# Kernel tuning notes

Hardware: AMD Instinct MI355X
Metric: run time of the kernel (lower is better)

Reference implementation:

```python
import jax, jax.numpy as jnp
import numpy as np

N, EN, NNZ, D, H = 100000, 25000, 200000, 128, 4
F = D  # out_channels per head (out_channels == embed_dim)
NEG_SLOPE = 0.2


def segment_softmax(logits, seg, num_segments):
    # numerically stable softmax over entries sharing the same segment id
    m = jax.ops.segment_max(logits, seg, num_segments=num_segments)
    ex = jnp.exp(logits - m[seg])
    s = jax.ops.segment_sum(ex, seg, num_segments=num_segments)
    return ex / s[seg]


def setup_inputs():
    key = jax.random.key(0)
    ks = jax.random.split(key, 10)
    X = jax.random.normal(ks[0], (N, D), jnp.float32)
    E = jax.random.normal(ks[1], (EN, D), jnp.float32)
    row = jax.random.randint(ks[2], (NNZ,), 0, N, dtype=jnp.int32)
    col = (jnp.arange(NNZ, dtype=jnp.int32) % EN)  # every hyperedge non-empty
    adj_index = jnp.stack([row, col])  # [2, nnz]
    adj_values = jax.random.uniform(ks[3], (NNZ,), jnp.float32) + 0.1
    s = 1.0 / np.sqrt(D)
    Wn = jax.random.normal(ks[4], (D, D), jnp.float32) * s
    bn = jnp.zeros((D,), jnp.float32)
    We = jax.random.normal(ks[5], (D, D), jnp.float32) * s
    be = jnp.zeros((D,), jnp.float32)
    Wlin = jax.random.normal(ks[6], (D, H * F), jnp.float32) * s
    att = jax.random.normal(ks[7], (1, H, 2 * F), jnp.float32) * s
    bias_conv = jnp.zeros((F,), jnp.float32)
    return {"X": X, "E": E, "adj_index": adj_index, "adj_values": adj_values,
            "Wn": Wn, "bn": bn, "We": We, "be": be, "Wlin": Wlin,
            "att": att, "bias_conv": bias_conv}


def reference(X, E, adj_index, adj_values, Wn, bn, We, be, Wlin, att, bias_conv):
    row, col = adj_index[0], adj_index[1]  # node idx, hyperedge idx

    # ---- compute_edge_feat: E_res = B^{-1} A^T (X Wn + bn) + (E We + be) + E
    edge_deg = jax.ops.segment_sum(adj_values, col, num_segments=EN)  # tsp.sum(A,0)
    norm_factor = 1.0 / edge_deg  # edges guaranteed non-empty
    X_trans = X @ Wn + bn
    agg = jax.ops.segment_sum(adj_values[:, None] * X_trans[row], col, num_segments=EN)
    E_res = norm_factor[:, None] * agg + (E @ We + be) + E

    # ---- HypergraphConv(use_attention=True, heads=H, concat=False), eval (dropout off)
    x = (X @ Wlin).reshape(N, H, F)
    e = (E_res @ Wlin).reshape(EN, H, F)
    x_i = x[row]           # [nnz, H, F]
    e_j = e[col]           # [nnz, H, F]
    alpha = (x_i * att[:, :, :F]).sum(-1) + (e_j * att[:, :, F:]).sum(-1)  # [nnz, H]
    alpha = jax.nn.leaky_relu(alpha, NEG_SLOPE)
    alpha = segment_softmax(alpha, row, N)  # softmax grouped by node index

    # degree normalizations D (nodes) and B (hyperedges)
    Dn = jax.ops.segment_sum(adj_values[col], row, num_segments=N)
    Dn = jnp.where(Dn > 0, 1.0 / Dn, 0.0)
    Bn = jax.ops.segment_sum(jnp.ones((NNZ,), x.dtype), col, num_segments=EN)
    Bn = jnp.where(Bn > 0, 1.0 / Bn, 0.0)

    # node -> hyperedge aggregation
    m1 = Bn[col][:, None, None] * x_i * alpha[:, :, None]
    out_e = jax.ops.segment_sum(m1, col, num_segments=EN)  # [EN, H, F]
    # hyperedge -> node aggregation
    m2 = Dn[row][:, None, None] * out_e[col] * alpha[:, :, None]
    out_n = jax.ops.segment_sum(m2, row, num_segments=N)   # [N, H, F]

    X_res = out_n.mean(axis=1) + bias_conv  # concat=False -> mean over heads + bias
    return (X_res, E_res)
```

## Files before the change

kernel.cpp:

```cpp
#include <hip/hip_runtime.h>

#define NN 100000
#define ENUM 25000
#define NNZ_C 200000

typedef __attribute__((ext_vector_type(8))) short bf16x8;
typedef __attribute__((ext_vector_type(4))) float f32x4;

__device__ __forceinline__ float blo(unsigned u) { return __uint_as_float(u << 16); }
__device__ __forceinline__ float bhi(unsigned u) { return __uint_as_float(u & 0xFFFF0000u); }
__device__ __forceinline__ unsigned short f2bf(float x) {
    unsigned u = __float_as_uint(x);
    unsigned r = (u + 0x7fff + ((u >> 16) & 1)) >> 16;
    return (unsigned short)r;
}
__device__ __forceinline__ unsigned pack2(float a, float b) {
    return (unsigned)f2bf(a) | ((unsigned)f2bf(b) << 16);
}
__device__ __forceinline__ void gload_lds16(const unsigned short* g, unsigned short* l) {
    __builtin_amdgcn_global_load_lds(
        (const __attribute__((address_space(1))) void*)g,
        (__attribute__((address_space(3))) void*)l, 16, 0, 0);
}

__global__ __launch_bounds__(256) void wtr_k(
    const float* __restrict__ W, unsigned short* __restrict__ Wt, int NC)
{
    const int t = blockIdx.x * 256 + threadIdx.x;
    if (t >= 128 * NC) return;
    const int c = t % NC, k = t / NC;
    const size_t pos = ((size_t)c * 128 + k) ^ ((c & 7) << 3);
    Wt[pos] = f2bf(W[t]);
}

__global__ __launch_bounds__(256) void wtr_big_k(
    const float* __restrict__ Wlin, unsigned short* __restrict__ WbigT)
{
    const int t = blockIdx.x * 256 + threadIdx.x;
    if (t >= 128 * 512) return;
    const int d = t >> 9, c512 = t & 511;
    const int h = c512 >> 7, f = c512 & 127;
    const int kk = d * 4 + h;
    const int kc = kk >> 7, dd = kk & 127;
    const size_t pos = (size_t)kc * 16384 + (((size_t)f * 128 + dd) ^ ((f & 7) << 3));
    WbigT[pos] = f2bf(Wlin[t]);
}

__global__ __launch_bounds__(256) void attw_k(
    const float* __restrict__ Wlin, const float* __restrict__ att,
    const float* __restrict__ bn, const float* __restrict__ be,
    float* __restrict__ A1, float* __restrict__ A2, float* __restrict__ bnbe)
{
    const int t = threadIdx.x;
    const int k = t & 127;
    const int pair = t >> 7;
    const float* wrow = Wlin + (size_t)k * 512;
    float s[4];
    #pragma unroll
    for (int h = 0; h < 4; h++) {
        float acc = 0.f;
        const float* ap = att + h * 256 + pair * 128;
        const float* wp = wrow + h * 128;
        for (int f = 0; f < 128; f++) acc += wp[f] * ap[f];
        s[h] = acc;
    }
    float* dst = (pair ? A2 : A1) + k * 4;
    dst[0] = s[0]; dst[1] = s[1]; dst[2] = s[2]; dst[3] = s[3];
    if (t < 128) bnbe[t] = bn[t] + be[t];
}

__global__ __launch_bounds__(256) void ax_k(
    const float* __restrict__ X, const float* __restrict__ A1,
    float* __restrict__ ax, int M)
{
    const int r = blockIdx.x * 4 + (threadIdx.x >> 6);
    const int lane = threadIdx.x & 63;
    if (r >= M) return;
    const int f0 = lane * 2;
    const float2 x = *(const float2*)(X + (size_t)r * 128 + f0);
    const float4 a0 = *(const float4*)(A1 + f0 * 4);
    const float4 a1 = *(const float4*)(A1 + f0 * 4 + 4);
    float s0 = x.x * a0.x + x.y * a1.x;
    float s1 = x.x * a0.y + x.y * a1.y;
    float s2 = x.x * a0.z + x.y * a1.z;
    float s3 = x.x * a0.w + x.y * a1.w;
    #pragma unroll
    for (int off = 1; off < 64; off <<= 1) {
        s0 += __shfl_xor(s0, off); s1 += __shfl_xor(s1, off);
        s2 += __shfl_xor(s2, off); s3 += __shfl_xor(s3, off);
    }
    if (lane == 0) *(float4*)(ax + (size_t)r * 4) = make_float4(s0, s1, s2, s3);
}

__global__ __launch_bounds__(256) void agg_k(
    const int* __restrict__ row, const float* __restrict__ adjv,
    const float* __restrict__ X, unsigned short* __restrict__ agg)
{
    const int e = blockIdx.x * 4 + (threadIdx.x >> 6);
    const int lane = threadIdx.x & 63;
    if (e >= ENUM) return;
    const int f0 = lane * 2;
    float a0 = 0.f, a1 = 0.f, deg = 0.f;
    #pragma unroll
    for (int j = 0; j < 8; j++) {
        const int k = e + j * ENUM;
        const float w = adjv[k];
        deg += w;
        const float2 x = *(const float2*)(X + (size_t)row[k] * 128 + f0);
        a0 += w * x.x; a1 += w * x.y;
    }
    const float rs = 1.f / deg;
    ((unsigned*)agg)[(size_t)e * 64 + lane] = pack2(a0 * rs, a1 * rs);
}

__global__ __launch_bounds__(256) void gemme_k(
    const unsigned short* __restrict__ agg, const float* __restrict__ E,
    const unsigned short* __restrict__ WnT, const unsigned short* __restrict__ WeT,
    const float* __restrict__ bnbe, float* __restrict__ Eres, int M)
{
    __shared__ unsigned short Ag[64 * 128];
    __shared__ unsigned short Ae[64 * 128];
    __shared__ unsigned short Bw[64 * 128];
    __shared__ unsigned short Bv[64 * 128];
    const int tid = threadIdx.x;
    const int r0 = blockIdx.x * 64;

    {
        int rr = tid >> 4;
        const int kc = (tid & 15) * 8;
        #pragma unroll
        for (int it = 0; it < 4; it++) {
            int r = r0 + rr; if (r > M - 1) r = M - 1;
            const uint4 vg = *(const uint4*)(agg + (size_t)r * 128 + kc);
            const float* ep = E + (size_t)r * 128 + kc;
            const float4 f0 = *(const float4*)ep;
            const float4 f1 = *(const float4*)(ep + 4);
            uint4 ve;
            ve.x = pack2(f0.x, f0.y); ve.y = pack2(f0.z, f0.w);
            ve.z = pack2(f1.x, f1.y); ve.w = pack2(f1.z, f1.w);
            const int idx = (rr * 128 + kc) ^ ((rr & 7) << 3);
            *(uint4*)&Ag[idx] = vg;
            *(uint4*)&Ae[idx] = ve;
            rr += 16;
        }
    }
    __syncthreads();

    const int lane = tid & 63;
    const int wid = tid >> 6;
    const int wr = wid >> 1, wc = wid & 1;
    const int fr = lane & 15;
    const int kg = (lane >> 4) * 8;

    bf16x8 ag[2][4], ae_[2][4];
    #pragma unroll
    for (int m = 0; m < 2; m++) {
        const int ar = wr * 32 + m * 16 + fr;
        #pragma unroll
        for (int ks = 0; ks < 4; ks++) {
            const int idx = (ar * 128 + ks * 32 + kg) ^ ((ar & 7) << 3);
            ag[m][ks] = *(const bf16x8*)&Ag[idx];
            ae_[m][ks] = *(const bf16x8*)&Ae[idx];
        }
    }

    for (int ct = 0; ct < 2; ct++) {
        __syncthreads();
        {
            const unsigned short* s1 = WnT + (size_t)ct * 8192 + tid * 8;
            const unsigned short* s2 = WeT + (size_t)ct * 8192 + tid * 8;
            unsigned short* d1 = &Bw[tid * 8];
            unsigned short* d2 = &Bv[tid * 8];
            #pragma unroll
            for (int it = 0; it < 4; it++) {
                gload_lds16(s1 + it * 2048, d1 + it * 2048);
                gload_lds16(s2 + it * 2048, d2 + it * 2048);
            }
        }
        __syncthreads();

        f32x4 acc[2][2] = {};
        #pragma unroll
        for (int ks = 0; ks < 4; ks++) {
            bf16x8 bw[2], bv[2];
            #pragma unroll
            for (int n = 0; n < 2; n++) {
                const int br = wc * 32 + n * 16 + fr;
                const int idx = (br * 128 + ks * 32 + kg) ^ ((br & 7) << 3);
                bw[n] = *(const bf16x8*)&Bw[idx];
                bv[n] = *(const bf16x8*)&Bv[idx];
            }
            #pragma unroll
            for (int m = 0; m < 2; m++)
                #pragma unroll
                for (int n = 0; n < 2; n++) {
                    acc[m][n] = __builtin_amdgcn_mfma_f32_16x16x32_bf16(ag[m][ks], bw[n], acc[m][n], 0, 0, 0);
                    acc[m][n] = __builtin_amdgcn_mfma_f32_16x16x32_bf16(ae_[m][ks], bv[n], acc[m][n], 0, 0, 0);
                }
        }

        #pragma unroll
        for (int m = 0; m < 2; m++) {
            #pragma unroll
            for (int n = 0; n < 2; n++) {
                const int c = ct * 64 + wc * 32 + n * 16 + fr;
                #pragma unroll
                for (int j = 0; j < 4; j++) {
                    const int r = r0 + wr * 32 + m * 16 + (lane >> 4) * 4 + j;
                    if (r < M)
                        Eres[(size_t)r * 128 + c] = acc[m][n][j] + bnbe[c] + E[(size_t)r * 128 + c];
                }
            }
        }
    }
}

__global__ __launch_bounds__(256) void ae_k(
    const float* __restrict__ Eres, const float* __restrict__ A2,
    float* __restrict__ ae)
{
    const int e = blockIdx.x * 4 + (threadIdx.x >> 6);
    const int lane = threadIdx.x & 63;
    if (e >= ENUM) return;
    const int f0 = lane * 2;
    const float2 v = *(const float2*)(Eres + (size_t)e * 128 + f0);
    const float4 a0 = *(const float4*)(A2 + f0 * 4);
    const float4 a1 = *(const float4*)(A2 + f0 * 4 + 4);
    float s0 = v.x * a0.x + v.y * a1.x;
    float s1 = v.x * a0.y + v.y * a1.y;
    float s2 = v.x * a0.z + v.y * a1.z;
    float s3 = v.x * a0.w + v.y * a1.w;
    #pragma unroll
    for (int off = 1; off < 64; off <<= 1) {
        s0 += __shfl_xor(s0, off); s1 += __shfl_xor(s1, off);
        s2 += __shfl_xor(s2, off); s3 += __shfl_xor(s3, off);
    }
    if (lane == 0) *(float4*)(ae + (size_t)e * 4) = make_float4(s0, s1, s2, s3);
}

__global__ __launch_bounds__(256) void zero_k(unsigned* __restrict__ p, int n)
{
    const int t = blockIdx.x * 256 + threadIdx.x;
    if (t < n) p[t] = 0u;
}

__global__ __launch_bounds__(256) void hist_k(
    const int* __restrict__ row, int* __restrict__ cnt)
{
    const int k = blockIdx.x * 256 + threadIdx.x;
    if (k < NNZ_C) atomicAdd(cnt + row[k], 1);
}

__global__ __launch_bounds__(256) void scan1_k(
    const int* __restrict__ cnt, int* __restrict__ rp, int* __restrict__ bsum, int n)
{
    __shared__ int sh[256];
    const int t = threadIdx.x, g = blockIdx.x * 256 + t;
    const int v = (g < n) ? cnt[g] : 0;
    sh[t] = v; __syncthreads();
    #pragma unroll
    for (int off = 1; off < 256; off <<= 1) {
        const int add = (t >= off) ? sh[t - off] : 0;
        __syncthreads();
        sh[t] += add;
        __syncthreads();
    }
    if (g < n) rp[g] = sh[t] - v;
    if (t == 255) bsum[blockIdx.x] = sh[255];
}

__global__ __launch_bounds__(512) void scan2_k(int* __restrict__ bsum, int nb)
{
    __shared__ int sh[512];
    const int t = threadIdx.x;
    const int v = (t < nb) ? bsum[t] : 0;
    sh[t] = v; __syncthreads();
    #pragma unroll
    for (int off = 1; off < 512; off <<= 1) {
        const int add = (t >= off) ? sh[t - off] : 0;
        __syncthreads();
        sh[t] += add;
        __syncthreads();
    }
    if (t < nb) bsum[t] = sh[t] - v;
}

__global__ __launch_bounds__(256) void scan3_k(
    int* __restrict__ rp, const int* __restrict__ bsum, int* __restrict__ cur, int n)
{
    const int g = blockIdx.x * 256 + threadIdx.x;
    if (g < n) {
        const int v = rp[g] + bsum[g >> 8];
        rp[g] = v;
        cur[g] = v;
    }
    if (g == 0) rp[n] = NNZ_C;
}

__global__ __launch_bounds__(256) void fill_k(
    const int* __restrict__ row, int* __restrict__ cur, int* __restrict__ eidx)
{
    const int k = blockIdx.x * 256 + threadIdx.x;
    if (k < NNZ_C) {
        const int p = atomicAdd(cur + row[k], 1);
        eidx[p] = k;
    }
}

__global__ __launch_bounds__(256) void softmax_csr_k(
    const int* __restrict__ rowptr, const int* __restrict__ eidx,
    const float* __restrict__ ax, const float* __restrict__ ae,
    float* __restrict__ alpha, float* __restrict__ alphag)
{
    const int r = blockIdx.x * 256 + threadIdx.x;
    if (r >= NN) return;
    const int p0 = rowptr[r], p1 = rowptr[r + 1];
    if (p0 == p1) return;
    const float4 axv = *(const float4*)(ax + (size_t)r * 4);

#define LRELU4(a) { a.x = (a.x >= 0.f) ? a.x : 0.2f * a.x;                    \
                    a.y = (a.y >= 0.f) ? a.y : 0.2f * a.y;                    \
                    a.z = (a.z >= 0.f) ? a.z : 0.2f * a.z;                    \
                    a.w = (a.w >= 0.f) ? a.w : 0.2f * a.w; }

    float4 m = make_float4(-1e30f, -1e30f, -1e30f, -1e30f);
    for (int p = p0; p < p1; ++p) {
        const int c = eidx[p] % ENUM;
        float4 a = *(const float4*)(ae + (size_t)c * 4);
        a.x += axv.x; a.y += axv.y; a.z += axv.z; a.w += axv.w;
        LRELU4(a);
        m.x = fmaxf(m.x, a.x); m.y = fmaxf(m.y, a.y);
        m.z = fmaxf(m.z, a.z); m.w = fmaxf(m.w, a.w);
    }
    float4 s = make_float4(0.f, 0.f, 0.f, 0.f);
    for (int p = p0; p < p1; ++p) {
        const int c = eidx[p] % ENUM;
        float4 a = *(const float4*)(ae + (size_t)c * 4);
        a.x += axv.x; a.y += axv.y; a.z += axv.z; a.w += axv.w;
        LRELU4(a);
        s.x += __expf(a.x - m.x); s.y += __expf(a.y - m.y);
        s.z += __expf(a.z - m.z); s.w += __expf(a.w - m.w);
    }
    const float4 rs = make_float4(1.f / s.x, 1.f / s.y, 1.f / s.z, 1.f / s.w);
    for (int p = p0; p < p1; ++p) {
        const int k = eidx[p];
        const int c = k % ENUM;
        float4 a = *(const float4*)(ae + (size_t)c * 4);
        a.x += axv.x; a.y += axv.y; a.z += axv.z; a.w += axv.w;
        LRELU4(a);
        float4 v;
        v.x = __expf(a.x - m.x) * rs.x; v.y = __expf(a.y - m.y) * rs.y;
        v.z = __expf(a.z - m.z) * rs.z; v.w = __expf(a.w - m.w) * rs.w;
        *(float4*)(alpha + ((size_t)k << 2)) = v;
        *(float4*)(alphag + ((size_t)p << 2)) = v;
    }
#undef LRELU4
}

__global__ __launch_bounds__(256) void aggx_k(
    const int* __restrict__ row, const float* __restrict__ alpha,
    const float* __restrict__ X, unsigned short* __restrict__ aggX)
{
    const int e = blockIdx.x * 4 + (threadIdx.x >> 6);
    const int lane = threadIdx.x & 63;
    if (e >= ENUM) return;
    const int f0 = lane * 2;
    float d0h0 = 0.f, d0h1 = 0.f, d0h2 = 0.f, d0h3 = 0.f;
    float d1h0 = 0.f, d1h1 = 0.f, d1h2 = 0.f, d1h3 = 0.f;
    #pragma unroll
    for (int j = 0; j < 8; j++) {
        const int k = e + j * ENUM;
        const float4 al = *(const float4*)(alpha + ((size_t)k << 2));
        const float2 x = *(const float2*)(X + (size_t)row[k] * 128 + f0);
        d0h0 += al.x * x.x; d0h1 += al.y * x.x; d0h2 += al.z * x.x; d0h3 += al.w * x.x;
        d1h0 += al.x * x.y; d1h1 += al.y * x.y; d1h2 += al.z * x.y; d1h3 += al.w * x.y;
    }
    uint4 o;
    o.x = pack2(0.125f * d0h0, 0.125f * d0h1);
    o.y = pack2(0.125f * d0h2, 0.125f * d0h3);
    o.z = pack2(0.125f * d1h0, 0.125f * d1h1);
    o.w = pack2(0.125f * d1h2, 0.125f * d1h3);
    *(uint4*)(aggX + (size_t)e * 512 + f0 * 4) = o;
}

__global__ __launch_bounds__(256) void aggn_k(
    const int* __restrict__ rowptr, const int* __restrict__ eidx,
    const float* __restrict__ adjv, const float* __restrict__ alphag,
    const unsigned short* __restrict__ aggX, unsigned short* __restrict__ aggN)
{
    const int r = blockIdx.x * 4 + (threadIdx.x >> 6);
    const int lane = threadIdx.x & 63;
    if (r >= NN) return;
    const int p0 = rowptr[r], p1 = rowptr[r + 1];
    const int f0 = lane * 2;
    float d0h0 = 0.f, d0h1 = 0.f, d0h2 = 0.f, d0h3 = 0.f;
    float d1h0 = 0.f, d1h1 = 0.f, d1h2 = 0.f, d1h3 = 0.f;
    float ds = 0.f;

#define AGN_BODY(P) {                                                         \
        const int c = eidx[P] % ENUM;                                         \
        ds += adjv[c];                                                        \
        const float4 al = *(const float4*)(alphag + ((size_t)(P) << 2));      \
        const uint4 u = *(const uint4*)(aggX + (size_t)c * 512 + f0 * 4);     \
        d0h0 += al.x * blo(u.x); d0h1 += al.y * bhi(u.x);                     \
        d0h2 += al.z * blo(u.y); d0h3 += al.w * bhi(u.y);                     \
        d1h0 += al.x * blo(u.z); d1h1 += al.y * bhi(u.z);                     \
        d1h2 += al.z * blo(u.w); d1h3 += al.w * bhi(u.w);                     \
    }

    int p = p0;
    for (; p + 2 <= p1; p += 2) { AGN_BODY(p); AGN_BODY(p + 1); }
    if (p < p1) AGN_BODY(p);
#undef AGN_BODY

    const float w = (p1 > p0) ? 0.25f / ds : 0.f;
    uint4 o;
    o.x = pack2(w * d0h0, w * d0h1);
    o.y = pack2(w * d0h2, w * d0h3);
    o.z = pack2(w * d1h0, w * d1h1);
    o.w = pack2(w * d1h2, w * d1h3);
    *(uint4*)(aggN + (size_t)r * 512 + f0 * 4) = o;
}

__global__ __launch_bounds__(256) void gemmf_k(
    const unsigned short* __restrict__ aggN, const unsigned short* __restrict__ WbigT,
    const float* __restrict__ bias, float* __restrict__ Xres, int M)
{
    __shared__ unsigned short As[64 * 128];
    __shared__ unsigned short Bs[128 * 128];
    const int tid = threadIdx.x;
    const int r0 = blockIdx.x * 64;
    const int lane = tid & 63;
    const int w = tid >> 6;
    const int wr = w >> 1, wc = w & 1;
    const int fr = lane & 15;
    const int kg = (lane >> 4) * 8;

    f32x4 acc[2][4] = {};

    for (int kc = 0; kc < 4; kc++) {
        __syncthreads();
        {
            int rr = tid >> 4;
            const int kcol = (tid & 15) * 8;
            #pragma unroll
            for (int it = 0; it < 4; it++) {
                int r = r0 + rr; if (r > M - 1) r = M - 1;
                const uint4 va = *(const uint4*)(aggN + (size_t)r * 512 + kc * 128 + kcol);
                *(uint4*)&As[(rr * 128 + kcol) ^ ((rr & 7) << 3)] = va;
                rr += 16;
            }
        }
        {
            const unsigned short* src = WbigT + (size_t)kc * 16384 + tid * 8;
            unsigned short* dst = &Bs[tid * 8];
            #pragma unroll
            for (int it = 0; it < 8; it++)
                gload_lds16(src + it * 2048, dst + it * 2048);
        }
        __syncthreads();

        #pragma unroll
        for (int ks = 0; ks < 4; ks++) {
            bf16x8 a[2], b[4];
            #pragma unroll
            for (int m = 0; m < 2; m++) {
                const int ar = wr * 32 + m * 16 + fr;
                a[m] = *(const bf16x8*)&As[(ar * 128 + ks * 32 + kg) ^ ((ar & 7) << 3)];
            }
            #pragma unroll
            for (int n = 0; n < 4; n++) {
                const int br = wc * 64 + n * 16 + fr;
                b[n] = *(const bf16x8*)&Bs[(br * 128 + ks * 32 + kg) ^ ((br & 7) << 3)];
            }
            #pragma unroll
            for (int m = 0; m < 2; m++)
                #pragma unroll
                for (int n = 0; n < 4; n++)
                    acc[m][n] = __builtin_amdgcn_mfma_f32_16x16x32_bf16(a[m], b[n], acc[m][n], 0, 0, 0);
        }
    }

    #pragma unroll
    for (int m = 0; m < 2; m++) {
        #pragma unroll
        for (int n = 0; n < 4; n++) {
            const int c = wc * 64 + n * 16 + fr;
            #pragma unroll
            for (int j = 0; j < 4; j++) {
                const int r = r0 + wr * 32 + m * 16 + (lane >> 4) * 4 + j;
                if (r < M)
                    Xres[(size_t)r * 128 + c] = acc[m][n][j] + bias[c];
            }
        }
    }
}

extern "C" void kernel_launch(void* const* d_in, const int* in_sizes, int n_in,
                              void* d_out, int out_size, void* d_ws, size_t ws_size,
                              hipStream_t stream)
{
    const float* X         = (const float*)d_in[0];
    const float* E         = (const float*)d_in[1];
    const int*   adj       = (const int*)d_in[2];
    const float* adjv      = (const float*)d_in[3];
    const float* Wn        = (const float*)d_in[4];
    const float* bn        = (const float*)d_in[5];
    const float* We        = (const float*)d_in[6];
    const float* be        = (const float*)d_in[7];
    const float* Wlin      = (const float*)d_in[8];
    const float* att       = (const float*)d_in[9];
    const float* bias_conv = (const float*)d_in[10];
    const int* row = adj;

    float* Xres = (float*)d_out;
    float* Eres = Xres + (size_t)NN * 128;

    char* wsb = (char*)d_ws;
    unsigned short* aggX  = (unsigned short*)(wsb);
    unsigned short* agg   = (unsigned short*)(wsb + 25600000);
    unsigned short* aggN  = (unsigned short*)(wsb + 51200000);
    unsigned short* WbigT = (unsigned short*)(wsb + 153600000);
    unsigned short* WnT   = (unsigned short*)(wsb + 153731072);
    unsigned short* WeT   = (unsigned short*)(wsb + 153763840);
    float* A1    = (float*)(wsb + 153796608);
    float* A2    = (float*)(wsb + 153798656);
    float* bnbe  = (float*)(wsb + 153800704);
    float* ax    = (float*)(wsb + 153802752);
    float* ae    = (float*)(wsb + 155402752);
    float* alpha = (float*)(wsb + 155802752);
    int* rowptr  = (int*)(wsb + 159002752);
    int* cnt     = (int*)(wsb + 159402768);
    int* eidx    = (int*)(wsb + 159802768);
    int* bsum    = (int*)(wsb + 160602768);
    float* alphag= (float*)(wsb + 160604816);

    zero_k<<<(NN + 255) / 256, 256, 0, stream>>>((unsigned*)cnt, NN);
    hist_k<<<(NNZ_C + 255) / 256, 256, 0, stream>>>(row, cnt);
    scan1_k<<<(NN + 255) / 256, 256, 0, stream>>>(cnt, rowptr, bsum, NN);
    scan2_k<<<1, 512, 0, stream>>>(bsum, (NN + 255) / 256);
    scan3_k<<<(NN + 255) / 256, 256, 0, stream>>>(rowptr, bsum, cnt, NN);
    fill_k<<<(NNZ_C + 255) / 256, 256, 0, stream>>>(row, cnt, eidx);

    wtr_big_k<<<256, 256, 0, stream>>>(Wlin, WbigT);
    wtr_k<<<64, 256, 0, stream>>>(Wn, WnT, 128);
    wtr_k<<<64, 256, 0, stream>>>(We, WeT, 128);
    attw_k<<<1, 256, 0, stream>>>(Wlin, att, bn, be, A1, A2, bnbe);

    ax_k<<<NN / 4, 256, 0, stream>>>(X, A1, ax, NN);

    agg_k<<<ENUM / 4, 256, 0, stream>>>(row, adjv, X, agg);
    gemme_k<<<391, 256, 0, stream>>>(agg, E, WnT, WeT, bnbe, Eres, ENUM);
    ae_k<<<ENUM / 4, 256, 0, stream>>>(Eres, A2, ae);

    softmax_csr_k<<<(NN + 255) / 256, 256, 0, stream>>>(rowptr, eidx, ax, ae, alpha, alphag);

    aggx_k<<<ENUM / 4, 256, 0, stream>>>(row, alpha, X, aggX);

    aggn_k<<<NN / 4, 256, 0, stream>>>(rowptr, eidx, adjv, alphag, aggX, aggN);

    gemmf_k<<<(NN + 63) / 64, 256, 0, stream>>>(aggN, WbigT, bias_conv, Xres, NN);
}
```

Before: 247.7 us.

## Fuse CSR hyperedge-to-node aggregation into final GEMM A-tile staging

Removes the separate aggn kernel and the 100MB bf16 aggN intermediate. The final GEMM now builds each A tile in shared memory by gathering aggX rows over the node's CSR neighbours, four threads per row, each handling 32 columns. This trades an intermediate write plus reread for gathers repeated inside each K chunk: eidx and alphag are reloaded four times, with extra register pressure from the 32-float accumulator and load imbalance within a block. Workspace offsets are compacted.

```diff
diff --git a/kernel.cpp b/kernel.cpp
--- a/kernel.cpp
+++ b/kernel.cpp
@@ -383,47 +383,10 @@
     *(uint4*)(aggX + (size_t)e * 512 + f0 * 4) = o;
 }
 
-__global__ __launch_bounds__(256) void aggn_k(
+__global__ __launch_bounds__(256) void aggn_gemmf_k(
     const int* __restrict__ rowptr, const int* __restrict__ eidx,
     const float* __restrict__ adjv, const float* __restrict__ alphag,
-    const unsigned short* __restrict__ aggX, unsigned short* __restrict__ aggN)
-{
-    const int r = blockIdx.x * 4 + (threadIdx.x >> 6);
-    const int lane = threadIdx.x & 63;
-    if (r >= NN) return;
-    const int p0 = rowptr[r], p1 = rowptr[r + 1];
-    const int f0 = lane * 2;
-    float d0h0 = 0.f, d0h1 = 0.f, d0h2 = 0.f, d0h3 = 0.f;
-    float d1h0 = 0.f, d1h1 = 0.f, d1h2 = 0.f, d1h3 = 0.f;
-    float ds = 0.f;
-
-#define AGN_BODY(P) {                                                         \
-        const int c = eidx[P] % ENUM;                                         \
-        ds += adjv[c];                                                        \
-        const float4 al = *(const float4*)(alphag + ((size_t)(P) << 2));      \
-        const uint4 u = *(const uint4*)(aggX + (size_t)c * 512 + f0 * 4);     \
-        d0h0 += al.x * blo(u.x); d0h1 += al.y * bhi(u.x);                     \
-        d0h2 += al.z * blo(u.y); d0h3 += al.w * bhi(u.y);                     \
-        d1h0 += al.x * blo(u.z); d1h1 += al.y * bhi(u.z);                     \
-        d1h2 += al.z * blo(u.w); d1h3 += al.w * bhi(u.w);                     \
-    }
-
-    int p = p0;
-    for (; p + 2 <= p1; p += 2) { AGN_BODY(p); AGN_BODY(p + 1); }
-    if (p < p1) AGN_BODY(p);
-#undef AGN_BODY
-
-    const float w = (p1 > p0) ? 0.25f / ds : 0.f;
-    uint4 o;
-    o.x = pack2(w * d0h0, w * d0h1);
-    o.y = pack2(w * d0h2, w * d0h3);
-    o.z = pack2(w * d1h0, w * d1h1);
-    o.w = pack2(w * d1h2, w * d1h3);
-    *(uint4*)(aggN + (size_t)r * 512 + f0 * 4) = o;
-}
-
-__global__ __launch_bounds__(256) void gemmf_k(
-    const unsigned short* __restrict__ aggN, const unsigned short* __restrict__ WbigT,
+    const unsigned short* __restrict__ aggX, const unsigned short* __restrict__ WbigT,
     const float* __restrict__ bias, float* __restrict__ Xres, int M)
 {
     __shared__ unsigned short As[64 * 128];
@@ -436,19 +399,51 @@
     const int fr = lane & 15;
     const int kg = (lane >> 4) * 8;
 
+    const int grow = tid >> 2;
+    const int gq = tid & 3;
+    int gp0 = 0, gp1 = 0;
+    float gw = 0.f;
+    {
+        const int r = r0 + grow;
+        if (r < M) {
+            gp0 = rowptr[r];
+            gp1 = rowptr[r + 1];
+            float ds = 0.f;
+            for (int p = gp0; p < gp1; ++p) ds += adjv[eidx[p] % ENUM];
+            gw = (gp1 > gp0) ? 0.25f / ds : 0.f;
+        }
+    }
+
     f32x4 acc[2][4] = {};
 
     for (int kc = 0; kc < 4; kc++) {
         __syncthreads();
+
         {
-            int rr = tid >> 4;
-            const int kcol = (tid & 15) * 8;
-            #pragma unroll
-            for (int it = 0; it < 4; it++) {
-                int r = r0 + rr; if (r > M - 1) r = M - 1;
-                const uint4 va = *(const uint4*)(aggN + (size_t)r * 512 + kc * 128 + kcol);
-                *(uint4*)&As[(rr * 128 + kcol) ^ ((rr & 7) << 3)] = va;
-                rr += 16;
+            float v[32];
+            #pragma unroll
+            for (int i = 0; i < 32; i++) v[i] = 0.f;
+            for (int p = gp0; p < gp1; ++p) {
+                const int c = eidx[p] % ENUM;
+                const float4 al = *(const float4*)(alphag + ((size_t)p << 2));
+                const unsigned short* src = aggX + (size_t)c * 512 + kc * 128 + gq * 32;
+                #pragma unroll
+                for (int i = 0; i < 32; i += 8) {
+                    const uint4 u = *(const uint4*)(src + i);
+                    v[i + 0] += al.x * blo(u.x); v[i + 1] += al.y * bhi(u.x);
+                    v[i + 2] += al.z * blo(u.y); v[i + 3] += al.w * bhi(u.y);
+                    v[i + 4] += al.x * blo(u.z); v[i + 5] += al.y * bhi(u.z);
+                    v[i + 6] += al.z * blo(u.w); v[i + 7] += al.w * bhi(u.w);
+                }
+            }
+            #pragma unroll
+            for (int i = 0; i < 32; i += 8) {
+                uint4 o;
+                o.x = pack2(gw * v[i + 0], gw * v[i + 1]);
+                o.y = pack2(gw * v[i + 2], gw * v[i + 3]);
+                o.z = pack2(gw * v[i + 4], gw * v[i + 5]);
+                o.w = pack2(gw * v[i + 6], gw * v[i + 7]);
+                *(uint4*)&As[(grow * 128 + gq * 32 + i) ^ ((grow & 7) << 3)] = o;
             }
         }
         {
@@ -519,21 +514,20 @@
     char* wsb = (char*)d_ws;
     unsigned short* aggX  = (unsigned short*)(wsb);
     unsigned short* agg   = (unsigned short*)(wsb + 25600000);
-    unsigned short* aggN  = (unsigned short*)(wsb + 51200000);
-    unsigned short* WbigT = (unsigned short*)(wsb + 153600000);
-    unsigned short* WnT   = (unsigned short*)(wsb + 153731072);
-    unsigned short* WeT   = (unsigned short*)(wsb + 153763840);
-    float* A1    = (float*)(wsb + 153796608);
-    float* A2    = (float*)(wsb + 153798656);
-    float* bnbe  = (float*)(wsb + 153800704);
-    float* ax    = (float*)(wsb + 153802752);
-    float* ae    = (float*)(wsb + 155402752);
-    float* alpha = (float*)(wsb + 155802752);
-    int* rowptr  = (int*)(wsb + 159002752);
-    int* cnt     = (int*)(wsb + 159402768);
-    int* eidx    = (int*)(wsb + 159802768);
-    int* bsum    = (int*)(wsb + 160602768);
-    float* alphag= (float*)(wsb + 160604816);
+    unsigned short* WbigT = (unsigned short*)(wsb + 32200000);
+    unsigned short* WnT   = (unsigned short*)(wsb + 32331072);
+    unsigned short* WeT   = (unsigned short*)(wsb + 32363840);
+    float* A1    = (float*)(wsb + 32396608);
+    float* A2    = (float*)(wsb + 32398656);
+    float* bnbe  = (float*)(wsb + 32400704);
+    float* ax    = (float*)(wsb + 32402752);
+    float* ae    = (float*)(wsb + 34002752);
+    float* alpha = (float*)(wsb + 34402752);
+    int* rowptr  = (int*)(wsb + 37602752);
+    int* cnt     = (int*)(wsb + 38002768);
+    int* eidx    = (int*)(wsb + 38402768);
+    int* bsum    = (int*)(wsb + 39202768);
+    float* alphag= (float*)(wsb + 39204816);
 
     zero_k<<<(NN + 255) / 256, 256, 0, stream>>>((unsigned*)cnt, NN);
     hist_k<<<(NNZ_C + 255) / 256, 256, 0, stream>>>(row, cnt);
@@ -557,7 +551,6 @@
 
     aggx_k<<<ENUM / 4, 256, 0, stream>>>(row, alpha, X, aggX);
 
-    aggn_k<<<NN / 4, 256, 0, stream>>>(rowptr, eidx, adjv, alphag, aggX, aggN);
-
-    gemmf_k<<<(NN + 63) / 64, 256, 0, stream>>>(aggN, WbigT, bias_conv, Xres, NN);
-}
+    aggn_gemmf_k<<<(NN + 63) / 64, 256, 0, stream>>>(
+        rowptr, eidx, adjv, alphag, aggX, WbigT, bias_conv, Xres, NN);
+}
```

Measured after the change: 256.6 us. 1.04x slower.

## Apply Wlin per head on hyperedges before gathering to nodes

Applied to the files above, without the earlier changes.

The per-head Wlin projection moves from after the node aggregation (a GEMM over 100k nodes with K=512) to before it, giving a per-head GEMM over 25k hyperedges that produces out_e in bf16. The node gather then reads the projected hyperedge features and sums the heads in registers, writing fp32 output plus bias directly. This removes the large aggN intermediate and the big node-side GEMM, at the cost of a wider gathered row per incidence and one more bf16 rounding step on out_e.

```diff
diff --git a/kernel.cpp b/kernel.cpp
--- a/kernel.cpp
+++ b/kernel.cpp
@@ -33,17 +33,15 @@
     Wt[pos] = f2bf(W[t]);
 }
 
-__global__ __launch_bounds__(256) void wtr_big_k(
-    const float* __restrict__ Wlin, unsigned short* __restrict__ WbigT)
+__global__ __launch_bounds__(256) void wtr_h_k(
+    const float* __restrict__ Wlin, unsigned short* __restrict__ WlinhT)
 {
     const int t = blockIdx.x * 256 + threadIdx.x;
     if (t >= 128 * 512) return;
     const int d = t >> 9, c512 = t & 511;
     const int h = c512 >> 7, f = c512 & 127;
-    const int kk = d * 4 + h;
-    const int kc = kk >> 7, dd = kk & 127;
-    const size_t pos = (size_t)kc * 16384 + (((size_t)f * 128 + dd) ^ ((f & 7) << 3));
-    WbigT[pos] = f2bf(Wlin[t]);
+    const size_t pos = (size_t)h * 16384 + (((size_t)f * 128 + d) ^ ((f & 7) << 3));
+    WlinhT[pos] = f2bf(Wlin[t]);
 }
 
 __global__ __launch_bounds__(256) void attw_k(
@@ -364,67 +362,29 @@
     const int e = blockIdx.x * 4 + (threadIdx.x >> 6);
     const int lane = threadIdx.x & 63;
     if (e >= ENUM) return;
-    const int f0 = lane * 2;
-    float d0h0 = 0.f, d0h1 = 0.f, d0h2 = 0.f, d0h3 = 0.f;
-    float d1h0 = 0.f, d1h1 = 0.f, d1h2 = 0.f, d1h3 = 0.f;
+    const int d0 = lane * 2;
+    float h0a = 0.f, h0b = 0.f, h1a = 0.f, h1b = 0.f;
+    float h2a = 0.f, h2b = 0.f, h3a = 0.f, h3b = 0.f;
     #pragma unroll
     for (int j = 0; j < 8; j++) {
         const int k = e + j * ENUM;
         const float4 al = *(const float4*)(alpha + ((size_t)k << 2));
-        const float2 x = *(const float2*)(X + (size_t)row[k] * 128 + f0);
-        d0h0 += al.x * x.x; d0h1 += al.y * x.x; d0h2 += al.z * x.x; d0h3 += al.w * x.x;
-        d1h0 += al.x * x.y; d1h1 += al.y * x.y; d1h2 += al.z * x.y; d1h3 += al.w * x.y;
-    }
-    uint4 o;
-    o.x = pack2(0.125f * d0h0, 0.125f * d0h1);
-    o.y = pack2(0.125f * d0h2, 0.125f * d0h3);
-    o.z = pack2(0.125f * d1h0, 0.125f * d1h1);
-    o.w = pack2(0.125f * d1h2, 0.125f * d1h3);
-    *(uint4*)(aggX + (size_t)e * 512 + f0 * 4) = o;
-}
-
-__global__ __launch_bounds__(256) void aggn_k(
-    const int* __restrict__ rowptr, const int* __restrict__ eidx,
-    const float* __restrict__ adjv, const float* __restrict__ alphag,
-    const unsigned short* __restrict__ aggX, unsigned short* __restrict__ aggN)
-{
-    const int r = blockIdx.x * 4 + (threadIdx.x >> 6);
-    const int lane = threadIdx.x & 63;
-    if (r >= NN) return;
-    const int p0 = rowptr[r], p1 = rowptr[r + 1];
-    const int f0 = lane * 2;
-    float d0h0 = 0.f, d0h1 = 0.f, d0h2 = 0.f, d0h3 = 0.f;
-    float d1h0 = 0.f, d1h1 = 0.f, d1h2 = 0.f, d1h3 = 0.f;
-    float ds = 0.f;
-
-#define AGN_BODY(P) {                                                         \
-        const int c = eidx[P] % ENUM;                                         \
-        ds += adjv[c];                                                        \
-        const float4 al = *(const float4*)(alphag + ((size_t)(P) << 2));      \
-        const uint4 u = *(const uint4*)(aggX + (size_t)c * 512 + f0 * 4);     \
-        d0h0 += al.x * blo(u.x); d0h1 += al.y * bhi(u.x);                     \
-        d0h2 += al.z * blo(u.y); d0h3 += al.w * bhi(u.y);                     \
-        d1h0 += al.x * blo(u.z); d1h1 += al.y * bhi(u.z);                     \
-        d1h2 += al.z * blo(u.w); d1h3 += al.w * bhi(u.w);                     \
-    }
-
-    int p = p0;
-    for (; p + 2 <= p1; p += 2) { AGN_BODY(p); AGN_BODY(p + 1); }
-    if (p < p1) AGN_BODY(p);
-#undef AGN_BODY
-
-    const float w = (p1 > p0) ? 0.25f / ds : 0.f;
-    uint4 o;
-    o.x = pack2(w * d0h0, w * d0h1);
-    o.y = pack2(w * d0h2, w * d0h3);
-    o.z = pack2(w * d1h0, w * d1h1);
-    o.w = pack2(w * d1h2, w * d1h3);
-    *(uint4*)(aggN + (size_t)r * 512 + f0 * 4) = o;
-}
-
-__global__ __launch_bounds__(256) void gemmf_k(
-    const unsigned short* __restrict__ aggN, const unsigned short* __restrict__ WbigT,
-    const float* __restrict__ bias, float* __restrict__ Xres, int M)
+        const float2 x = *(const float2*)(X + (size_t)row[k] * 128 + d0);
+        h0a += al.x * x.x; h0b += al.x * x.y;
+        h1a += al.y * x.x; h1b += al.y * x.y;
+        h2a += al.z * x.x; h2b += al.z * x.y;
+        h3a += al.w * x.x; h3b += al.w * x.y;
+    }
+    unsigned* dst = (unsigned*)aggX + (size_t)e * 256 + lane;
+    dst[0]   = pack2(0.125f * h0a, 0.125f * h0b);
+    dst[64]  = pack2(0.125f * h1a, 0.125f * h1b);
+    dst[128] = pack2(0.125f * h2a, 0.125f * h2b);
+    dst[192] = pack2(0.125f * h3a, 0.125f * h3b);
+}
+
+__global__ __launch_bounds__(256) void gemmoe_k(
+    const unsigned short* __restrict__ aggX, const unsigned short* __restrict__ WlinhT,
+    unsigned short* __restrict__ out_e, int M)
 {
     __shared__ unsigned short As[64 * 128];
     __shared__ unsigned short Bs[128 * 128];
@@ -436,23 +396,21 @@
     const int fr = lane & 15;
     const int kg = (lane >> 4) * 8;
 
-    f32x4 acc[2][4] = {};
-
-    for (int kc = 0; kc < 4; kc++) {
+    for (int h = 0; h < 4; h++) {
         __syncthreads();
         {
             int rr = tid >> 4;
-            const int kcol = (tid & 15) * 8;
+            const int kc = (tid & 15) * 8;
             #pragma unroll
             for (int it = 0; it < 4; it++) {
                 int r = r0 + rr; if (r > M - 1) r = M - 1;
-                const uint4 va = *(const uint4*)(aggN + (size_t)r * 512 + kc * 128 + kcol);
-                *(uint4*)&As[(rr * 128 + kcol) ^ ((rr & 7) << 3)] = va;
+                const uint4 va = *(const uint4*)(aggX + (size_t)r * 512 + h * 128 + kc);
+                *(uint4*)&As[(rr * 128 + kc) ^ ((rr & 7) << 3)] = va;
                 rr += 16;
             }
         }
         {
-            const unsigned short* src = WbigT + (size_t)kc * 16384 + tid * 8;
+            const unsigned short* src = WlinhT + (size_t)h * 16384 + tid * 8;
             unsigned short* dst = &Bs[tid * 8];
             #pragma unroll
             for (int it = 0; it < 8; it++)
@@ -460,6 +418,7 @@
         }
         __syncthreads();
 
+        f32x4 acc[2][4] = {};
         #pragma unroll
         for (int ks = 0; ks < 4; ks++) {
             bf16x8 a[2], b[4];
@@ -479,21 +438,56 @@
                 for (int n = 0; n < 4; n++)
                     acc[m][n] = __builtin_amdgcn_mfma_f32_16x16x32_bf16(a[m], b[n], acc[m][n], 0, 0, 0);
         }
-    }
-
-    #pragma unroll
-    for (int m = 0; m < 2; m++) {
+
         #pragma unroll
-        for (int n = 0; n < 4; n++) {
-            const int c = wc * 64 + n * 16 + fr;
-            #pragma unroll
-            for (int j = 0; j < 4; j++) {
-                const int r = r0 + wr * 32 + m * 16 + (lane >> 4) * 4 + j;
-                if (r < M)
-                    Xres[(size_t)r * 128 + c] = acc[m][n][j] + bias[c];
-            }
-        }
-    }
+        for (int m = 0; m < 2; m++) {
+            #pragma unroll
+            for (int n = 0; n < 4; n++) {
+                const int c = wc * 64 + n * 16 + fr;
+                #pragma unroll
+                for (int j = 0; j < 4; j++) {
+                    const int r = r0 + wr * 32 + m * 16 + (lane >> 4) * 4 + j;
+                    if (r < M)
+                        out_e[(size_t)r * 512 + h * 128 + c] = f2bf(acc[m][n][j]);
+                }
+            }
+        }
+    }
+}
+
+__global__ __launch_bounds__(256) void xgather_k(
+    const int* __restrict__ rowptr, const int* __restrict__ eidx,
+    const float* __restrict__ adjv, const float* __restrict__ alphag,
+    const unsigned short* __restrict__ out_e, const float* __restrict__ bias,
+    float* __restrict__ Xres)
+{
+    const int r = blockIdx.x * 4 + (threadIdx.x >> 6);
+    const int lane = threadIdx.x & 63;
+    if (r >= NN) return;
+    const int p0 = rowptr[r], p1 = rowptr[r + 1];
+    const int f0 = lane * 2;
+    float a0 = 0.f, a1 = 0.f, ds = 0.f;
+
+#define XG_BODY(P) {                                                          \
+        const int c = eidx[P] % ENUM;                                         \
+        ds += adjv[c];                                                        \
+        const float4 al = *(const float4*)(alphag + ((size_t)(P) << 2));      \
+        const unsigned* ob = (const unsigned*)out_e + (size_t)c * 256 + lane; \
+        const unsigned u0 = ob[0], u1 = ob[64], u2 = ob[128], u3 = ob[192];   \
+        a0 += al.x * blo(u0) + al.y * blo(u1) + al.z * blo(u2) + al.w * blo(u3); \
+        a1 += al.x * bhi(u0) + al.y * bhi(u1) + al.z * bhi(u2) + al.w * bhi(u3); \
+    }
+
+    int p = p0;
+    for (; p + 2 <= p1; p += 2) { XG_BODY(p); XG_BODY(p + 1); }
+    if (p < p1) XG_BODY(p);
+#undef XG_BODY
+
+    const float w = (p1 > p0) ? 0.25f / ds : 0.f;
+    float2 o;
+    o.x = bias[f0] + w * a0;
+    o.y = bias[f0 + 1] + w * a1;
+    *(float2*)(Xres + (size_t)r * 128 + f0) = o;
 }
 
 extern "C" void kernel_launch(void* const* d_in, const int* in_sizes, int n_in,
@@ -518,22 +512,22 @@
 
     char* wsb = (char*)d_ws;
     unsigned short* aggX  = (unsigned short*)(wsb);
-    unsigned short* agg   = (unsigned short*)(wsb + 25600000);
-    unsigned short* aggN  = (unsigned short*)(wsb + 51200000);
-    unsigned short* WbigT = (unsigned short*)(wsb + 153600000);
-    unsigned short* WnT   = (unsigned short*)(wsb + 153731072);
-    unsigned short* WeT   = (unsigned short*)(wsb + 153763840);
-    float* A1    = (float*)(wsb + 153796608);
-    float* A2    = (float*)(wsb + 153798656);
-    float* bnbe  = (float*)(wsb + 153800704);
-    float* ax    = (float*)(wsb + 153802752);
-    float* ae    = (float*)(wsb + 155402752);
-    float* alpha = (float*)(wsb + 155802752);
-    int* rowptr  = (int*)(wsb + 159002752);
-    int* cnt     = (int*)(wsb + 159402768);
-    int* eidx    = (int*)(wsb + 159802768);
-    int* bsum    = (int*)(wsb + 160602768);
-    float* alphag= (float*)(wsb + 160604816);
+    unsigned short* out_e = (unsigned short*)(wsb + 25600000);
+    unsigned short* agg   = (unsigned short*)(wsb + 51200000);
+    unsigned short* WlinhT= (unsigned short*)(wsb + 57800000);
+    unsigned short* WnT   = (unsigned short*)(wsb + 57931072);
+    unsigned short* WeT   = (unsigned short*)(wsb + 57963840);
+    float* A1    = (float*)(wsb + 57996608);
+    float* A2    = (float*)(wsb + 57998656);
+    float* bnbe  = (float*)(wsb + 58000704);
+    float* ax    = (float*)(wsb + 58002752);
+    float* ae    = (float*)(wsb + 59602752);
+    float* alpha = (float*)(wsb + 60002752);
+    int* rowptr  = (int*)(wsb + 63202752);
+    int* cnt     = (int*)(wsb + 63602768);
+    int* eidx    = (int*)(wsb + 64002768);
+    int* bsum    = (int*)(wsb + 64802768);
+    float* alphag= (float*)(wsb + 64804816);
 
     zero_k<<<(NN + 255) / 256, 256, 0, stream>>>((unsigned*)cnt, NN);
     hist_k<<<(NNZ_C + 255) / 256, 256, 0, stream>>>(row, cnt);
@@ -542,7 +536,7 @@
     scan3_k<<<(NN + 255) / 256, 256, 0, stream>>>(rowptr, bsum, cnt, NN);
     fill_k<<<(NNZ_C + 255) / 256, 256, 0, stream>>>(row, cnt, eidx);
 
-    wtr_big_k<<<256, 256, 0, stream>>>(Wlin, WbigT);
+    wtr_h_k<<<256, 256, 0, stream>>>(Wlin, WlinhT);
     wtr_k<<<64, 256, 0, stream>>>(Wn, WnT, 128);
     wtr_k<<<64, 256, 0, stream>>>(We, WeT, 128);
     attw_k<<<1, 256, 0, stream>>>(Wlin, att, bn, be, A1, A2, bnbe);
@@ -557,7 +551,7 @@
 
     aggx_k<<<ENUM / 4, 256, 0, stream>>>(row, alpha, X, aggX);
 
-    aggn_k<<<NN / 4, 256, 0, stream>>>(rowptr, eidx, adjv, alphag, aggX, aggN);
-
-    gemmf_k<<<(NN + 63) / 64, 256, 0, stream>>>(aggN, WbigT, bias_conv, Xres, NN);
-}
+    gemmoe_k<<<(ENUM + 63) / 64, 256, 0, stream>>>(aggX, WlinhT, out_e, ENUM);
+
+    xgather_k<<<NN / 4, 256, 0, stream>>>(rowptr, eidx, adjv, alphag, out_e, bias_conv, Xres);
+}
```

New measurement: 215.0 us. 1.15x faster.
